# Kernel tuning notes

Hardware: AMD Instinct MI355X
Metric: run time of the kernel (lower is better)

The kernel has to match this reference:

```python
import jax, jax.numpy as jnp
import numpy as np

D_MODEL = 1024
NUM_HEADS = 16
D_K = D_MODEL // NUM_HEADS  # 64
THETA = 10000.0
MAX_SEQ_LEN = 2048


def _trunc_normal(key, shape, std):
    # approximate trunc_normal_(mean=0, std, a=-3*std, b=3*std)
    u = jax.random.truncated_normal(key, -3.0, 3.0, shape, dtype=jnp.float32)
    return u * std


def setup_inputs() -> dict:
    key = jax.random.key(0)
    ks = jax.random.split(key, 5)
    x = jax.random.normal(ks[0], (2, 2048, D_MODEL), dtype=jnp.float32)
    token_positions = jnp.arange(2048, dtype=jnp.int64 if jax.config.jax_enable_x64 else jnp.int32)
    sigma = 2.0 / (D_MODEL + D_MODEL)
    Wq = _trunc_normal(ks[1], (D_MODEL, D_MODEL), sigma)
    Wk = _trunc_normal(ks[2], (D_MODEL, D_MODEL), sigma)
    Wv = _trunc_normal(ks[3], (D_MODEL, D_MODEL), sigma)
    Wo = _trunc_normal(ks[4], (D_MODEL, D_MODEL), sigma)
    return {"in_features": x, "Wq": Wq, "Wk": Wk, "Wv": Wv, "Wo": Wo,
            "token_positions": token_positions}


def _rope(x, cos_phi, sin_phi):
    # x: (..., seq, d_k); cos/sin: (seq, d_k//2)
    x_even = x[..., 0::2]
    x_odd = x[..., 1::2]
    y_even = x_even * cos_phi - x_odd * sin_phi
    y_odd = x_even * sin_phi + x_odd * cos_phi
    # interleave back
    y = jnp.stack([y_even, y_odd], axis=-1)
    return y.reshape(x.shape)


def reference(in_features, Wq, Wk, Wv, Wo, token_positions):
    b, s, d = in_features.shape
    h, dk = NUM_HEADS, D_K
    # projections: weight is (d_out, d_in)
    q = jnp.einsum('bsd,ed->bse', in_features, Wq)
    k = jnp.einsum('bsd,ed->bse', in_features, Wk)
    v = jnp.einsum('bsd,ed->bse', in_features, Wv)
    # split heads: (b, h, s, dk)
    q = q.reshape(b, s, h, dk).transpose(0, 2, 1, 3)
    k = k.reshape(b, s, h, dk).transpose(0, 2, 1, 3)
    v = v.reshape(b, s, h, dk).transpose(0, 2, 1, 3)
    # RoPE tables
    inv_freq = 1.0 / (THETA ** (jnp.arange(0, dk, 2, dtype=jnp.float32) / dk))
    phi = token_positions.astype(jnp.float32)[:, None] * inv_freq[None, :]  # (s, dk/2)
    cos_phi, sin_phi = jnp.cos(phi), jnp.sin(phi)
    q = _rope(q, cos_phi, sin_phi)
    k = _rope(k, cos_phi, sin_phi)
    # causal mask
    mask = jnp.tril(jnp.ones((s, s), dtype=bool))
    scores = jnp.einsum('bhqd,bhkd->bhqk', q, k) / jnp.sqrt(jnp.float32(dk))
    scores = jnp.where(mask, scores, -jnp.inf)
    attn = jax.nn.softmax(scores, axis=-1)
    out = jnp.einsum('bhqk,bhkd->bhqd', attn, v)
    out = out.transpose(0, 2, 1, 3).reshape(b, s, d)
    return jnp.einsum('bsd,ed->bse', out, Wo)
```

## Files before the change

### kernel.cpp

```cpp
#include <hip/hip_runtime.h>
#include <hip/hip_bf16.h>
#include <math.h>

#define S_  2048
#define DM_ 1024

typedef unsigned short u16;
typedef __attribute__((ext_vector_type(8))) short short8;
typedef __attribute__((ext_vector_type(4))) float f32x4;

__device__ __forceinline__ u16 f2bf(float f) {
  unsigned u = __float_as_uint(f);
  u += 0x7fffu + ((u >> 16) & 1u);
  return (u16)(u >> 16);
}
__device__ __forceinline__ float bf2f(u16 h) {
  return __uint_as_float((unsigned)h << 16);
}
__device__ __forceinline__ unsigned pack_bf2(float a, float b) {
  union { __hip_bfloat162 h2; unsigned u; } cv;
  cv.h2 = __float22bfloat162_rn(float2{a, b});
  return cv.u;
}
__device__ __forceinline__ void cp16(const void* g, void* l) {
  __builtin_amdgcn_global_load_lds(
      (const __attribute__((address_space(1))) unsigned*)(uintptr_t)g,
      (__attribute__((address_space(3))) unsigned*)(unsigned)(uintptr_t)l, 16, 0, 0);
}

struct CastArgs { const float* src[5]; u16* dst[5]; int n[5]; };

__global__ __launch_bounds__(256) void cast_kernel(CastArgs a) {
  const int z = blockIdx.y;
  const int i = (blockIdx.x * 256 + threadIdx.x) * 8;
  if (i >= a.n[z]) return;
  const float4* s = (const float4*)(a.src[z] + i);
  float4 v0 = s[0], v1 = s[1];
  short8 r;
  r[0] = (short)f2bf(v0.x); r[1] = (short)f2bf(v0.y);
  r[2] = (short)f2bf(v0.z); r[3] = (short)f2bf(v0.w);
  r[4] = (short)f2bf(v1.x); r[5] = (short)f2bf(v1.y);
  r[6] = (short)f2bf(v1.z); r[7] = (short)f2bf(v1.w);
  *(short8*)(a.dst[z] + i) = r;
}

struct GemmArgs { const u16* A; const u16* W[3]; void* out[3]; int modes; };

template<int BN, int MINW, int GXL>
__global__ __launch_bounds__(256, MINW) void gemm_mfma(GemmArgs g) {
  constexpr int BM = 128;
  constexpr int NW = BN / 32;
  constexpr int RBB = BN / 32;
  constexpr int ABYTES = BM * 64 * 2;
  constexpr int SLOT = ABYTES + BN * 64 * 2;
  __shared__ __align__(16) char lds[2 * SLOT];

  const int tid = threadIdx.x, lane = tid & 63, w = tid >> 6;
  const int wm = w >> 1, wn = w & 1;
  const int t = lane & 15, u = lane >> 4;
  const int l3 = lane >> 3, l7 = lane & 7;
  const int z = blockIdx.z;

  const int nwg = (int)gridDim.y << GXL;
  const int flat = (int)blockIdx.x + ((int)blockIdx.y << GXL);
  const int swz = (flat & 7) * (nwg >> 3) + (flat >> 3);
  const int m0 = (swz >> GXL) * BM;
  const int n0 = (swz & ((1 << GXL) - 1)) * BN;

  const u16* __restrict__ A = g.A;
  const u16* __restrict__ W = g.W[z];

  const int axor = l7 << 4;
  const int ksw = (l7 ^ l3) * 8;
  const u16* Ab = A + (size_t)(m0 + l3) * 1024 + ksw;
  const u16* Wb = W + (size_t)(n0 + l3) * 1024 + ksw;

  auto stg = [&](int kt) {
    char* sb = lds + (kt & 1) * SLOT;
    #pragma unroll
    for (int r = 0; r < 4; r++)
      cp16(Ab + (size_t)(w * 4 + r) * 8192 + kt * 64, sb + (w * 4 + r) * 1024);
    #pragma unroll
    for (int r = 0; r < RBB; r++)
      cp16(Wb + (size_t)(w * RBB + r) * 8192 + kt * 64, sb + ABYTES + (w * RBB + r) * 1024);
  };

  const f32x4 fz = {0.f, 0.f, 0.f, 0.f};
  f32x4 acc[4][NW];
  #pragma unroll
  for (int i = 0; i < 4; i++)
    #pragma unroll
    for (int j = 0; j < NW; j++) acc[i][j] = fz;

  stg(0);
  asm volatile("s_waitcnt vmcnt(0)" ::: "memory");
  __builtin_amdgcn_s_barrier();

  for (int kt = 0; kt < 16; kt++) {
    const char* cs = lds + (kt & 1) * SLOT;
    if (kt < 15) stg(kt + 1);

    short8 af[2][4], bfr[2][NW];
    #pragma unroll
    for (int ks = 0; ks < 2; ks++) {
      const int co = (ks * 64 + u * 16) ^ axor;
      const char* ap = cs + (wm * 64 + t) * 128 + co;
      const char* bp = cs + ABYTES + (wn * (BN / 2) + t) * 128 + co;
      #pragma unroll
      for (int mf = 0; mf < 4; mf++) af[ks][mf] = *(const short8*)(ap + mf * 2048);
      #pragma unroll
      for (int nf = 0; nf < NW; nf++) bfr[ks][nf] = *(const short8*)(bp + nf * 2048);
    }
    asm volatile("s_waitcnt lgkmcnt(0)" ::: "memory");
    __builtin_amdgcn_sched_barrier(0);
    __builtin_amdgcn_s_setprio(1);
    #pragma unroll
    for (int ks = 0; ks < 2; ks++)
      #pragma unroll
      for (int mf = 0; mf < 4; mf++)
        #pragma unroll
        for (int nf = 0; nf < NW; nf++)
          acc[mf][nf] = __builtin_amdgcn_mfma_f32_16x16x32_bf16(af[ks][mf], bfr[ks][nf], acc[mf][nf], 0, 0, 0);
    __builtin_amdgcn_s_setprio(0);

    asm volatile("s_waitcnt vmcnt(0)" ::: "memory");
    __builtin_amdgcn_s_barrier();
  }

  const int mode = (g.modes >> (2 * z)) & 3;
  const int rbase = m0 + wm * 64 + u * 4;
  const int cbase = n0 + wn * (BN / 2) + t;
  if (mode == 0) {
    u16* O = (u16*)g.out[z];
    #pragma unroll
    for (int mt = 0; mt < 4; mt++)
      #pragma unroll
      for (int nt = 0; nt < NW; nt++)
        #pragma unroll
        for (int r = 0; r < 4; r++)
          O[(size_t)(rbase + mt * 16 + r) * 1024 + cbase + nt * 16] = f2bf(acc[mt][nt][r]);
  } else if (mode == 1) {
    u16* O = (u16*)g.out[z];
    #pragma unroll
    for (int mt = 0; mt < 4; mt++)
      #pragma unroll
      for (int nt = 0; nt < NW; nt++) {
        int gr = rbase + mt * 16;
        int b = gr >> 11, s0 = gr & (S_ - 1);
        int gc = cbase + nt * 16;
        int h = gc >> 6, d = gc & 63;
        ushort4 v;
        v.x = f2bf(acc[mt][nt][0]); v.y = f2bf(acc[mt][nt][1]);
        v.z = f2bf(acc[mt][nt][2]); v.w = f2bf(acc[mt][nt][3]);
        *(ushort4*)&O[(size_t)((b * 16 + h) * 64 + d) * 2048 + s0] = v;
      }
  } else {
    float* O = (float*)g.out[z];
    #pragma unroll
    for (int mt = 0; mt < 4; mt++)
      #pragma unroll
      for (int nt = 0; nt < NW; nt++)
        #pragma unroll
        for (int r = 0; r < 4; r++)
          O[(size_t)(rbase + mt * 16 + r) * 1024 + cbase + nt * 16] = acc[mt][nt][r];
  }
}

__global__ __launch_bounds__(256) void rope_kernel(u16* qb, u16* kb, const int* __restrict__ tp) {
  const int isq = (blockIdx.y == 0);
  u16* p = isq ? qb : kb;
  const float outscale = isq ? 0.18033688011112042f : 1.0f;
  const int i = (blockIdx.x * 256 + threadIdx.x) * 8;
  const int s = (i >> 10) & (S_ - 1);
  const int d = i & 63;
  const float pos = (float)tp[s];
  short8 v = *(short8*)(p + i);
  #pragma unroll
  for (int j = 0; j < 4; j++) {
    float inv = exp2f(-(float)(d + 2 * j) * 0.20762050593046439f);
    float phi = pos * inv;
    float sn, cs;
    sincosf(phi, &sn, &cs);
    float xe = bf2f((u16)v[2 * j]), xo = bf2f((u16)v[2 * j + 1]);
    v[2 * j]     = (short)f2bf((xe * cs - xo * sn) * outscale);
    v[2 * j + 1] = (short)f2bf((xe * sn + xo * cs) * outscale);
  }
  *(short8*)(p + i) = v;
}

__global__ __launch_bounds__(512, 4) void attn_mfma(const u16* __restrict__ qb, const u16* __restrict__ kb,
                                                    const u16* __restrict__ vt, u16* __restrict__ ab) {
  __shared__ __align__(16) u16 Qs[2][4096];
  __shared__ __align__(16) u16 Ks[2][4096];
  __shared__ __align__(16) u16 Vs[2][4096];

  const int tid = threadIdx.x, lane = tid & 63, w = tid >> 6;
  const int v = w & 3, g = w >> 2;
  const int t = lane & 15, u = lane >> 4;
  const int bh = blockIdx.y, b = bh >> 4, h = bh & 15;
  const int i = blockIdx.x;
  const int qa = 31 - i;
  const int qbt = i;
  const int nk = 32 - i;
  const size_t qkb = (size_t)b * S_ * 1024 + h * 64;
  const size_t vtb = (size_t)bh * 64 * 2048;

  {
    const int qtile = g ? qbt : qa;
    cp16(qb + qkb + (size_t)(qtile * 64 + lane) * 1024 + v * 8,       (char*)Qs[g] + v * 1024);
    cp16(qb + qkb + (size_t)(qtile * 64 + lane) * 1024 + (v + 4) * 8, (char*)Qs[g] + 4096 + v * 1024);
  }
  cp16(kb + qkb + (size_t)lane * 1024 + w * 8, (char*)Ks[0] + w * 1024);
  cp16(vt + vtb + (size_t)lane * 2048 + w * 8, (char*)Vs[0] + w * 1024);
  __syncthreads();

  short8 aqA[2], aqP[2];
  #pragma unroll
  for (int ks = 0; ks < 2; ks++) {
    aqA[ks] = *(const short8*)((const char*)Qs[0] + (ks * 4 + u) * 1024 + (v * 16 + t) * 16);
    short8 bq = *(const short8*)((const char*)Qs[1] + (ks * 4 + u) * 1024 + (v * 16 + t) * 16);
    aqP[ks] = g ? bq : aqA[ks];
  }

  const f32x4 fzero = {0.f, 0.f, 0.f, 0.f};
  f32x4 oPrim[4], oSec[4];
  #pragma unroll
  for (int ct = 0; ct < 4; ct++) { oPrim[ct] = fzero; oSec[ct] = fzero; }
  float rsumP = 0.f, rsumS = 0.f;

  const int qprim = g ? qbt : qa;
  const int qrowP = qprim * 64 + v * 16 + t;
  const int qrowA = qa * 64 + v * 16 + t;

  for (int kt = 0; kt < nk; kt++) {
    const int cur = kt & 1, nxt = cur ^ 1;
    if (kt + 1 < nk) {
      cp16(kb + qkb + (size_t)((kt + 1) * 64 + lane) * 1024 + w * 8, (char*)Ks[nxt] + w * 1024);
      cp16(vt + vtb + (size_t)lane * 2048 + (kt + 1) * 64 + w * 8,   (char*)Vs[nxt] + w * 1024);
    }

    if (kt <= qbt) {
      f32x4 st[4] = {fzero, fzero, fzero, fzero};
      #pragma unroll
      for (int ks = 0; ks < 2; ks++)
        #pragma unroll
        for (int ct = 0; ct < 4; ct++) {
          short8 kf = *(const short8*)((const char*)Ks[cur] + (ks * 4 + u) * 1024 + (ct * 16 + t) * 16);
          st[ct] = __builtin_amdgcn_mfma_f32_16x16x32_bf16(kf, aqP[ks], st[ct], 0, 0, 0);
        }

      unsigned pb2[4][2];
      const bool diag = (kt == qprim);
      #pragma unroll
      for (int ct = 0; ct < 4; ct++) {
        float p[4];
        #pragma unroll
        for (int r = 0; r < 4; r++) {
          int key = kt * 64 + ct * 16 + 4 * u + r;
          float pv = exp2f(st[ct][r]);
          p[r] = (diag && key > qrowP) ? 0.f : pv;
          rsumP += p[r];
        }
        pb2[ct][0] = pack_bf2(p[0], p[1]);
        pb2[ct][1] = pack_bf2(p[2], p[3]);
      }

      #pragma unroll
      for (int ks = 0; ks < 2; ks++) {
        union { short8 s8; int i4[4]; } pf;
        #pragma unroll
        for (int jj = 0; jj < 4; jj++) {
          int src = 32 * (u & 1) + 16 * (jj >> 1) + t;
          int v0 = __shfl((int)pb2[ks * 2][jj & 1], src, 64);
          int v1 = __shfl((int)pb2[ks * 2 + 1][jj & 1], src, 64);
          pf.i4[jj] = (u >> 1) ? v1 : v0;
        }
        #pragma unroll
        for (int ct = 0; ct < 4; ct++) {
          short8 vf = *(const short8*)((const char*)Vs[cur] + (ks * 4 + u) * 1024 + (ct * 16 + t) * 16);
          oPrim[ct] = __builtin_amdgcn_mfma_f32_16x16x32_bf16(vf, pf.s8, oPrim[ct], 0, 0, 0);
        }
      }
    } else {
      f32x4 st2[2] = {fzero, fzero};
      #pragma unroll
      for (int ks = 0; ks < 2; ks++)
        #pragma unroll
        for (int c = 0; c < 2; c++) {
          short8 kf = *(const short8*)((const char*)Ks[cur] + (ks * 4 + u) * 1024 + ((2 * g + c) * 16 + t) * 16);
          st2[c] = __builtin_amdgcn_mfma_f32_16x16x32_bf16(kf, aqA[ks], st2[c], 0, 0, 0);
        }

      unsigned ph[2][2];
      float rs = 0.f;
      const bool diag = (kt == qa);
      #pragma unroll
      for (int c = 0; c < 2; c++) {
        float p[4];
        #pragma unroll
        for (int r = 0; r < 4; r++) {
          int key = kt * 64 + (2 * g + c) * 16 + 4 * u + r;
          float pv = exp2f(st2[c][r]);
          p[r] = (diag && key > qrowA) ? 0.f : pv;
          rs += p[r];
        }
        ph[c][0] = pack_bf2(p[0], p[1]);
        ph[c][1] = pack_bf2(p[2], p[3]);
      }

      union { short8 s8; int i4[4]; } pf;
      #pragma unroll
      for (int jj = 0; jj < 4; jj++) {
        int src = 32 * (u & 1) + 16 * (jj >> 1) + t;
        int v0 = __shfl((int)ph[0][jj & 1], src, 64);
        int v1 = __shfl((int)ph[1][jj & 1], src, 64);
        pf.i4[jj] = (u >> 1) ? v1 : v0;
      }
      if (g) {
        rsumS += rs;
        #pragma unroll
        for (int ct = 0; ct < 4; ct++) {
          short8 vf = *(const short8*)((const char*)Vs[cur] + (4 + u) * 1024 + (ct * 16 + t) * 16);
          oSec[ct] = __builtin_amdgcn_mfma_f32_16x16x32_bf16(vf, pf.s8, oSec[ct], 0, 0, 0);
        }
      } else {
        rsumP += rs;
        #pragma unroll
        for (int ct = 0; ct < 4; ct++) {
          short8 vf = *(const short8*)((const char*)Vs[cur] + u * 1024 + (ct * 16 + t) * 16);
          oPrim[ct] = __builtin_amdgcn_mfma_f32_16x16x32_bf16(vf, pf.s8, oPrim[ct], 0, 0, 0);
        }
      }
    }
    __syncthreads();
  }

  float* dmpO = (float*)Ks;
  float* dmpR = (float*)Vs;
  if (g) {
    #pragma unroll
    for (int ct = 0; ct < 4; ct++)
      *(f32x4*)&dmpO[(size_t)(v * 64 + lane) * 16 + ct * 4] = oSec[ct];
    dmpR[v * 64 + lane] = rsumS;
    float rs = rsumP;
    rs += __shfl_xor(rs, 16, 64);
    rs += __shfl_xor(rs, 32, 64);
    const float inv = 1.0f / rs;
    #pragma unroll
    for (int ct = 0; ct < 4; ct++) {
      ushort4 vv;
      vv.x = f2bf(oPrim[ct][0] * inv); vv.y = f2bf(oPrim[ct][1] * inv);
      vv.z = f2bf(oPrim[ct][2] * inv); vv.w = f2bf(oPrim[ct][3] * inv);
      *(ushort4*)&ab[((size_t)b * S_ + qrowP) * 1024 + h * 64 + ct * 16 + 4 * u] = vv;
    }
  }
  __syncthreads();
  if (!g) {
    #pragma unroll
    for (int ct = 0; ct < 4; ct++) {
      f32x4 add = *(const f32x4*)&dmpO[(size_t)(v * 64 + lane) * 16 + ct * 4];
      oPrim[ct] += add;
    }
    float rs = rsumP + dmpR[v * 64 + lane];
    rs += __shfl_xor(rs, 16, 64);
    rs += __shfl_xor(rs, 32, 64);
    const float inv = 1.0f / rs;
    #pragma unroll
    for (int ct = 0; ct < 4; ct++) {
      ushort4 vv;
      vv.x = f2bf(oPrim[ct][0] * inv); vv.y = f2bf(oPrim[ct][1] * inv);
      vv.z = f2bf(oPrim[ct][2] * inv); vv.w = f2bf(oPrim[ct][3] * inv);
      *(ushort4*)&ab[((size_t)b * S_ + qrowA) * 1024 + h * 64 + ct * 16 + 4 * u] = vv;
    }
  }
}

extern "C" void kernel_launch(void* const* d_in, const int* in_sizes, int n_in,
                              void* d_out, int out_size, void* d_ws, size_t ws_size,
                              hipStream_t stream) {
  const float* x  = (const float*)d_in[0];
  const float* Wq = (const float*)d_in[1];
  const float* Wk = (const float*)d_in[2];
  const float* Wv = (const float*)d_in[3];
  const float* Wo = (const float*)d_in[4];
  const int*   tp = (const int*)d_in[5];
  float* out = (float*)d_out;

  char* ws = (char*)d_ws;
  u16* xb  = (u16*)(ws);
  u16* wqb = (u16*)(ws + (8 << 20));
  u16* wkb = (u16*)(ws + (10 << 20));
  u16* wvb = (u16*)(ws + (12 << 20));
  u16* wob = (u16*)(ws + (14 << 20));
  u16* qbuf = (u16*)(ws + (16 << 20));
  u16* kbuf = (u16*)(ws + (24 << 20));
  u16* vtb  = (u16*)(ws + (32 << 20));
  u16* abuf = (u16*)(ws + (40 << 20));

  CastArgs ca;
  ca.src[0] = x;  ca.dst[0] = xb;  ca.n[0] = 2 * S_ * DM_;
  ca.src[1] = Wq; ca.dst[1] = wqb; ca.n[1] = DM_ * DM_;
  ca.src[2] = Wk; ca.dst[2] = wkb; ca.n[2] = DM_ * DM_;
  ca.src[3] = Wv; ca.dst[3] = wvb; ca.n[3] = DM_ * DM_;
  ca.src[4] = Wo; ca.dst[4] = wob; ca.n[4] = DM_ * DM_;
  cast_kernel<<<dim3(2048, 5), 256, 0, stream>>>(ca);

  GemmArgs gq;
  gq.A = xb;
  gq.W[0] = wqb; gq.W[1] = wkb; gq.W[2] = wvb;
  gq.out[0] = qbuf; gq.out[1] = kbuf; gq.out[2] = vtb;
  gq.modes = (1 << 4);
  gemm_mfma<128, 2, 3><<<dim3(8, 32, 3), 256, 0, stream>>>(gq);

  rope_kernel<<<dim3(2048, 2), 256, 0, stream>>>(qbuf, kbuf, tp);

  attn_mfma<<<dim3(16, 32), 512, 0, stream>>>(qbuf, kbuf, vtb, abuf);

  GemmArgs go;
  go.A = abuf;
  go.W[0] = wob; go.W[1] = wob; go.W[2] = wob;
  go.out[0] = out; go.out[1] = out; go.out[2] = out;
  go.modes = 2;
  gemm_mfma<64, 3, 4><<<dim3(16, 32, 1), 256, 0, stream>>>(go);
}
```

Baseline: 186.3 us.

## Triple-buffer GEMM loads, shrink QKV tile to 64, split diag masking in attention

The GEMM kernel now uses three LDS stages and prefetches two k-tiles ahead, with a partial vmcnt wait so loads overlap compute. BN is fixed at 64, which doubles the QKV GEMM grid and raises its parallelism, while the output GEMM drops from 3 to 2 waves-per-SIMD occupancy hint. In the attention kernel, the causal-mask check is moved into a separate diagonal-only branch so off-diagonal tiles skip the compare, and MFMA sections are wrapped in setprio. Risks are higher LDS use, which may lower occupancy, and less A-tile reuse in the QKV GEMM.

```diff
diff --git a/kernel.cpp b/kernel.cpp
--- a/kernel.cpp
+++ b/kernel.cpp
@@ -46,14 +46,12 @@
 
 struct GemmArgs { const u16* A; const u16* W[3]; void* out[3]; int modes; };
 
-template<int BN, int MINW, int GXL>
-__global__ __launch_bounds__(256, MINW) void gemm_mfma(GemmArgs g) {
-  constexpr int BM = 128;
-  constexpr int NW = BN / 32;
-  constexpr int RBB = BN / 32;
+template<int GXL>
+__global__ __launch_bounds__(256, 2) void gemm_mfma(GemmArgs g) {
+  constexpr int BM = 128, BN = 64;
   constexpr int ABYTES = BM * 64 * 2;
   constexpr int SLOT = ABYTES + BN * 64 * 2;
-  __shared__ __align__(16) char lds[2 * SLOT];
+  __shared__ __align__(16) char lds[3 * SLOT];
 
   const int tid = threadIdx.x, lane = tid & 63, w = tid >> 6;
   const int wm = w >> 1, wn = w & 1;
@@ -75,41 +73,40 @@
   const u16* Ab = A + (size_t)(m0 + l3) * 1024 + ksw;
   const u16* Wb = W + (size_t)(n0 + l3) * 1024 + ksw;
 
-  auto stg = [&](int kt) {
-    char* sb = lds + (kt & 1) * SLOT;
+  auto stg = [&](char* sb, int kt) {
     #pragma unroll
     for (int r = 0; r < 4; r++)
       cp16(Ab + (size_t)(w * 4 + r) * 8192 + kt * 64, sb + (w * 4 + r) * 1024);
     #pragma unroll
-    for (int r = 0; r < RBB; r++)
-      cp16(Wb + (size_t)(w * RBB + r) * 8192 + kt * 64, sb + ABYTES + (w * RBB + r) * 1024);
+    for (int r = 0; r < 2; r++)
+      cp16(Wb + (size_t)(w * 2 + r) * 8192 + kt * 64, sb + ABYTES + (w * 2 + r) * 1024);
   };
 
   const f32x4 fz = {0.f, 0.f, 0.f, 0.f};
-  f32x4 acc[4][NW];
+  f32x4 acc[4][2];
   #pragma unroll
-  for (int i = 0; i < 4; i++)
-    #pragma unroll
-    for (int j = 0; j < NW; j++) acc[i][j] = fz;
-
-  stg(0);
-  asm volatile("s_waitcnt vmcnt(0)" ::: "memory");
+  for (int i = 0; i < 4; i++) { acc[i][0] = fz; acc[i][1] = fz; }
+
+  stg(lds, 0);
+  stg(lds + SLOT, 1);
+  asm volatile("s_waitcnt vmcnt(6)" ::: "memory");
   __builtin_amdgcn_s_barrier();
 
+  int rs_ = 0, ss_ = 2;
   for (int kt = 0; kt < 16; kt++) {
-    const char* cs = lds + (kt & 1) * SLOT;
-    if (kt < 15) stg(kt + 1);
-
-    short8 af[2][4], bfr[2][NW];
+    const char* cs = lds + rs_ * SLOT;
+    if (kt + 2 < 16) stg(lds + ss_ * SLOT, kt + 2);
+
+    short8 af[2][4], bfr[2][2];
     #pragma unroll
     for (int ks = 0; ks < 2; ks++) {
       const int co = (ks * 64 + u * 16) ^ axor;
       const char* ap = cs + (wm * 64 + t) * 128 + co;
-      const char* bp = cs + ABYTES + (wn * (BN / 2) + t) * 128 + co;
+      const char* bp = cs + ABYTES + (wn * 32 + t) * 128 + co;
       #pragma unroll
       for (int mf = 0; mf < 4; mf++) af[ks][mf] = *(const short8*)(ap + mf * 2048);
       #pragma unroll
-      for (int nf = 0; nf < NW; nf++) bfr[ks][nf] = *(const short8*)(bp + nf * 2048);
+      for (int nf = 0; nf < 2; nf++) bfr[ks][nf] = *(const short8*)(bp + nf * 2048);
     }
     asm volatile("s_waitcnt lgkmcnt(0)" ::: "memory");
     __builtin_amdgcn_sched_barrier(0);
@@ -119,23 +116,26 @@
       #pragma unroll
       for (int mf = 0; mf < 4; mf++)
         #pragma unroll
-        for (int nf = 0; nf < NW; nf++)
+        for (int nf = 0; nf < 2; nf++)
           acc[mf][nf] = __builtin_amdgcn_mfma_f32_16x16x32_bf16(af[ks][mf], bfr[ks][nf], acc[mf][nf], 0, 0, 0);
     __builtin_amdgcn_s_setprio(0);
 
-    asm volatile("s_waitcnt vmcnt(0)" ::: "memory");
+    if (kt + 2 < 16)      { asm volatile("s_waitcnt vmcnt(6)" ::: "memory"); }
+    else if (kt + 1 < 16) { asm volatile("s_waitcnt vmcnt(0)" ::: "memory"); }
     __builtin_amdgcn_s_barrier();
+    rs_ = (rs_ == 2) ? 0 : rs_ + 1;
+    ss_ = (ss_ == 2) ? 0 : ss_ + 1;
   }
 
   const int mode = (g.modes >> (2 * z)) & 3;
   const int rbase = m0 + wm * 64 + u * 4;
-  const int cbase = n0 + wn * (BN / 2) + t;
+  const int cbase = n0 + wn * 32 + t;
   if (mode == 0) {
     u16* O = (u16*)g.out[z];
     #pragma unroll
     for (int mt = 0; mt < 4; mt++)
       #pragma unroll
-      for (int nt = 0; nt < NW; nt++)
+      for (int nt = 0; nt < 2; nt++)
         #pragma unroll
         for (int r = 0; r < 4; r++)
           O[(size_t)(rbase + mt * 16 + r) * 1024 + cbase + nt * 16] = f2bf(acc[mt][nt][r]);
@@ -144,7 +144,7 @@
     #pragma unroll
     for (int mt = 0; mt < 4; mt++)
       #pragma unroll
-      for (int nt = 0; nt < NW; nt++) {
+      for (int nt = 0; nt < 2; nt++) {
         int gr = rbase + mt * 16;
         int b = gr >> 11, s0 = gr & (S_ - 1);
         int gc = cbase + nt * 16;
@@ -159,7 +159,7 @@
     #pragma unroll
     for (int mt = 0; mt < 4; mt++)
       #pragma unroll
-      for (int nt = 0; nt < NW; nt++)
+      for (int nt = 0; nt < 2; nt++)
         #pragma unroll
         for (int r = 0; r < 4; r++)
           O[(size_t)(rbase + mt * 16 + r) * 1024 + cbase + nt * 16] = acc[mt][nt][r];
@@ -241,6 +241,7 @@
 
     if (kt <= qbt) {
       f32x4 st[4] = {fzero, fzero, fzero, fzero};
+      __builtin_amdgcn_s_setprio(1);
       #pragma unroll
       for (int ks = 0; ks < 2; ks++)
         #pragma unroll
@@ -248,21 +249,33 @@
           short8 kf = *(const short8*)((const char*)Ks[cur] + (ks * 4 + u) * 1024 + (ct * 16 + t) * 16);
           st[ct] = __builtin_amdgcn_mfma_f32_16x16x32_bf16(kf, aqP[ks], st[ct], 0, 0, 0);
         }
+      __builtin_amdgcn_s_setprio(0);
 
       unsigned pb2[4][2];
-      const bool diag = (kt == qprim);
-      #pragma unroll
-      for (int ct = 0; ct < 4; ct++) {
-        float p[4];
-        #pragma unroll
-        for (int r = 0; r < 4; r++) {
-          int key = kt * 64 + ct * 16 + 4 * u + r;
-          float pv = exp2f(st[ct][r]);
-          p[r] = (diag && key > qrowP) ? 0.f : pv;
-          rsumP += p[r];
-        }
-        pb2[ct][0] = pack_bf2(p[0], p[1]);
-        pb2[ct][1] = pack_bf2(p[2], p[3]);
+      if (kt == qprim) {
+        #pragma unroll
+        for (int ct = 0; ct < 4; ct++) {
+          float p[4];
+          #pragma unroll
+          for (int r = 0; r < 4; r++) {
+            int key = kt * 64 + ct * 16 + 4 * u + r;
+            float pv = exp2f(st[ct][r]);
+            p[r] = (key > qrowP) ? 0.f : pv;
+          }
+          rsumP += (p[0] + p[1]) + (p[2] + p[3]);
+          pb2[ct][0] = pack_bf2(p[0], p[1]);
+          pb2[ct][1] = pack_bf2(p[2], p[3]);
+        }
+      } else {
+        #pragma unroll
+        for (int ct = 0; ct < 4; ct++) {
+          float p[4];
+          #pragma unroll
+          for (int r = 0; r < 4; r++) p[r] = exp2f(st[ct][r]);
+          rsumP += (p[0] + p[1]) + (p[2] + p[3]);
+          pb2[ct][0] = pack_bf2(p[0], p[1]);
+          pb2[ct][1] = pack_bf2(p[2], p[3]);
+        }
       }
 
       #pragma unroll
@@ -275,14 +288,17 @@
           int v1 = __shfl((int)pb2[ks * 2 + 1][jj & 1], src, 64);
           pf.i4[jj] = (u >> 1) ? v1 : v0;
         }
+        __builtin_amdgcn_s_setprio(1);
         #pragma unroll
         for (int ct = 0; ct < 4; ct++) {
           short8 vf = *(const short8*)((const char*)Vs[cur] + (ks * 4 + u) * 1024 + (ct * 16 + t) * 16);
           oPrim[ct] = __builtin_amdgcn_mfma_f32_16x16x32_bf16(vf, pf.s8, oPrim[ct], 0, 0, 0);
         }
+        __builtin_amdgcn_s_setprio(0);
       }
     } else {
       f32x4 st2[2] = {fzero, fzero};
+      __builtin_amdgcn_s_setprio(1);
       #pragma unroll
       for (int ks = 0; ks < 2; ks++)
         #pragma unroll
@@ -290,22 +306,34 @@
           short8 kf = *(const short8*)((const char*)Ks[cur] + (ks * 4 + u) * 1024 + ((2 * g + c) * 16 + t) * 16);
           st2[c] = __builtin_amdgcn_mfma_f32_16x16x32_bf16(kf, aqA[ks], st2[c], 0, 0, 0);
         }
+      __builtin_amdgcn_s_setprio(0);
 
       unsigned ph[2][2];
       float rs = 0.f;
-      const bool diag = (kt == qa);
-      #pragma unroll
-      for (int c = 0; c < 2; c++) {
-        float p[4];
-        #pragma unroll
-        for (int r = 0; r < 4; r++) {
-          int key = kt * 64 + (2 * g + c) * 16 + 4 * u + r;
-          float pv = exp2f(st2[c][r]);
-          p[r] = (diag && key > qrowA) ? 0.f : pv;
-          rs += p[r];
-        }
-        ph[c][0] = pack_bf2(p[0], p[1]);
-        ph[c][1] = pack_bf2(p[2], p[3]);
+      if (kt == qa) {
+        #pragma unroll
+        for (int c = 0; c < 2; c++) {
+          float p[4];
+          #pragma unroll
+          for (int r = 0; r < 4; r++) {
+            int key = kt * 64 + (2 * g + c) * 16 + 4 * u + r;
+            float pv = exp2f(st2[c][r]);
+            p[r] = (key > qrowA) ? 0.f : pv;
+          }
+          rs += (p[0] + p[1]) + (p[2] + p[3]);
+          ph[c][0] = pack_bf2(p[0], p[1]);
+          ph[c][1] = pack_bf2(p[2], p[3]);
+        }
+      } else {
+        #pragma unroll
+        for (int c = 0; c < 2; c++) {
+          float p[4];
+          #pragma unroll
+          for (int r = 0; r < 4; r++) p[r] = exp2f(st2[c][r]);
+          rs += (p[0] + p[1]) + (p[2] + p[3]);
+          ph[c][0] = pack_bf2(p[0], p[1]);
+          ph[c][1] = pack_bf2(p[2], p[3]);
+        }
       }
 
       union { short8 s8; int i4[4]; } pf;
@@ -318,18 +346,22 @@
       }
       if (g) {
         rsumS += rs;
+        __builtin_amdgcn_s_setprio(1);
         #pragma unroll
         for (int ct = 0; ct < 4; ct++) {
           short8 vf = *(const short8*)((const char*)Vs[cur] + (4 + u) * 1024 + (ct * 16 + t) * 16);
           oSec[ct] = __builtin_amdgcn_mfma_f32_16x16x32_bf16(vf, pf.s8, oSec[ct], 0, 0, 0);
         }
+        __builtin_amdgcn_s_setprio(0);
       } else {
         rsumP += rs;
+        __builtin_amdgcn_s_setprio(1);
         #pragma unroll
         for (int ct = 0; ct < 4; ct++) {
           short8 vf = *(const short8*)((const char*)Vs[cur] + u * 1024 + (ct * 16 + t) * 16);
           oPrim[ct] = __builtin_amdgcn_mfma_f32_16x16x32_bf16(vf, pf.s8, oPrim[ct], 0, 0, 0);
         }
+        __builtin_amdgcn_s_setprio(0);
       }
     }
     __syncthreads();
@@ -410,7 +442,7 @@
   gq.W[0] = wqb; gq.W[1] = wkb; gq.W[2] = wvb;
   gq.out[0] = qbuf; gq.out[1] = kbuf; gq.out[2] = vtb;
   gq.modes = (1 << 4);
-  gemm_mfma<128, 2, 3><<<dim3(8, 32, 3), 256, 0, stream>>>(gq);
+  gemm_mfma<4><<<dim3(16, 32, 3), 256, 0, stream>>>(gq);
 
   rope_kernel<<<dim3(2048, 2), 256, 0, stream>>>(qbuf, kbuf, tp);
 
@@ -421,5 +453,5 @@
   go.W[0] = wob; go.W[1] = wob; go.W[2] = wob;
   go.out[0] = out; go.out[1] = out; go.out[2] = out;
   go.modes = 2;
-  gemm_mfma<64, 3, 4><<<dim3(16, 32, 1), 256, 0, stream>>>(go);
-}
+  gemm_mfma<4><<<dim3(16, 32, 1), 256, 0, stream>>>(go);
+}
```

Result: no change. 183.9 us (-1.3%).
